# Optimization experiments

Measured on AMD Instinct MI355X. Metric: run time of the kernel, lower is better.

## Reference

```python
import jax, jax.numpy as jnp
import numpy as np


def log_g(x):
    # log of g(x) = x + 0.5 if x >= 0 else sigmoid(x)  (minGRU paper Appendix B)
    return jnp.where(x >= 0, jnp.log(jax.nn.relu(x) + 0.5), -jax.nn.softplus(-x))


def parallel_scan_log(log_coeffs, log_values):
    # log_coeffs: [B, T, H]; log_values: [B, T+1, H]
    a_star = jnp.pad(jnp.cumsum(log_coeffs, axis=1), ((0, 0), (1, 0), (0, 0)))  # [B, T+1, H]
    log_h = a_star + jax.lax.cumlogsumexp(log_values - a_star, axis=1)
    return jnp.exp(log_h)  # [B, T+1, H]


def setup_inputs() -> dict:
    key = jax.random.key(0)
    ks = jax.random.split(key, 6)
    B, T, D, H = 4, 4096, 1024, 1024
    scale = 1.0 / np.sqrt(D)
    return {
        "x": jax.random.normal(ks[0], (B, T, D), dtype=jnp.float32),
        "h_0": jax.random.uniform(ks[1], (B, H), dtype=jnp.float32),
        "Wz": jax.random.normal(ks[2], (H, D), dtype=jnp.float32) * scale,
        "bz": jnp.zeros((H,), dtype=jnp.float32),
        "Wh": jax.random.normal(ks[3], (H, D), dtype=jnp.float32) * scale,
        "bh": jnp.zeros((H,), dtype=jnp.float32),
    }


def reference(x, h_0, Wz, bz, Wh, bh):
    T = x.shape[1]
    k = jnp.einsum("btd,hd->bth", x, Wz) + bz          # linear_z(x)
    log_z = -jax.nn.softplus(-k)                          # log sigmoid(k)
    log_coeffs = -jax.nn.softplus(k)                      # log (1 - sigmoid(k))
    log_h_0 = log_g(h_0)[:, None, :]                      # [B, 1, H]
    log_tilde_h = log_g(jnp.einsum("btd,hd->bth", x, Wh) + bh)
    log_values = jnp.concatenate([log_h_0, log_z + log_tilde_h], axis=1)  # [B, T+1, H]
    h = parallel_scan_log(log_coeffs, log_values)
    return h[:, -T:, :]
```

## Files before the change

### kernel.cpp

```cpp
#include <hip/hip_runtime.h>
#include <hip/hip_bf16.h>
#include <hip/hip_fp16.h>

#define B_ 4
#define T_ 4096
#define D_ 1024
#define H_ 1024
#define M_ (B_ * T_)

typedef __attribute__((ext_vector_type(8))) short short8;
typedef __attribute__((ext_vector_type(4))) float f32x4;

__device__ __forceinline__ unsigned short f2bf(float f) {
    unsigned int u = __float_as_uint(f);
    u += 0x7fffu + ((u >> 16) & 1u);
    return (unsigned short)(u >> 16);
}

__global__ __launch_bounds__(256) void convert_all(
    const float* __restrict__ x, const float* __restrict__ wz, const float* __restrict__ wh,
    unsigned short* __restrict__ xb, unsigned short* __restrict__ wzb, unsigned short* __restrict__ whb)
{
    int i = blockIdx.x * 256 + threadIdx.x;
    const float* s; unsigned short* d; int off;
    if (i < 4194304)      { s = x;  d = xb;  off = i; }
    else if (i < 4456448) { s = wz; d = wzb; off = i - 4194304; }
    else                  { s = wh; d = whb; off = i - 4456448; }
    float4 f = ((const float4*)s)[off];
    ushort4 u;
    u.x = f2bf(f.x); u.y = f2bf(f.y); u.z = f2bf(f.z); u.w = f2bf(f.w);
    ((ushort4*)d)[off] = u;
}

__device__ __forceinline__ void async16(const void* g, void* l) {
    __builtin_amdgcn_global_load_lds(
        (__attribute__((address_space(1))) void*)g,
        (__attribute__((address_space(3))) void*)l,
        16, 0, 0);
}

__global__ __launch_bounds__(256, 4) void dual_gemm_kernel(
    const unsigned short* __restrict__ xb,
    const unsigned short* __restrict__ wzb,
    const unsigned short* __restrict__ whb,
    const float* __restrict__ bz,
    const float* __restrict__ bh,
    __half2* __restrict__ av16,
    float2* __restrict__ chunkAV)
{
    __shared__ short8 ldsA[8 * 64];
    __shared__ short8 ldsBz[4 * 64];
    __shared__ short8 ldsBh[4 * 64];

    const int tid   = threadIdx.x;
    const int lane  = tid & 63;
    const int w     = __builtin_amdgcn_readfirstlane(tid >> 6);
    const int whalf = w >> 1;
    const int nhalf = w & 1;
    const int nb    = blockIdx.x >> 7;
    const int mb    = blockIdx.x & 127;
    const int r16   = lane & 15;
    const int q     = lane >> 4;

    const int laneoff = r16 * D_ + q * 8;

    const unsigned short* gA0 = xb  + (size_t)(mb * 128 + (2 * w) * 16) * D_ + laneoff;
    const unsigned short* gA1 = gA0 + 16 * D_;
    const unsigned short* gBz = wzb + (size_t)(nb * 64 + w * 16) * D_ + laneoff;
    const unsigned short* gBh = whb + (size_t)(nb * 64 + w * 16) * D_ + laneoff;
    short8* lA0 = &ldsA[(2 * w) * 64];
    short8* lA1 = &ldsA[(2 * w + 1) * 64];
    short8* lBz = &ldsBz[w * 64];
    short8* lBh = &ldsBh[w * 64];

    f32x4 accz[4][2] = {};
    f32x4 acch[4][2] = {};

    for (int kk = 0; kk < D_; kk += 32) {
        __syncthreads();
        async16(gA0 + kk, lA0);
        async16(gA1 + kk, lA1);
        async16(gBz + kk, lBz);
        async16(gBh + kk, lBh);
        __syncthreads();

        short8 fa[4], fz[2], fh[2];
#pragma unroll
        for (int gm = 0; gm < 4; ++gm) fa[gm] = ldsA[(whalf * 4 + gm) * 64 + lane];
#pragma unroll
        for (int gn = 0; gn < 2; ++gn) {
            fz[gn] = ldsBz[(nhalf * 2 + gn) * 64 + lane];
            fh[gn] = ldsBh[(nhalf * 2 + gn) * 64 + lane];
        }
#pragma unroll
        for (int gm = 0; gm < 4; ++gm)
#pragma unroll
            for (int gn = 0; gn < 2; ++gn) {
                accz[gm][gn] = __builtin_amdgcn_mfma_f32_16x16x32_bf16(fa[gm], fz[gn], accz[gm][gn], 0, 0, 0);
                acch[gm][gn] = __builtin_amdgcn_mfma_f32_16x16x32_bf16(fa[gm], fh[gn], acch[gm][gn], 0, 0, 0);
            }
    }

    const int cglob = mb * 2 + whalf;
    const int cc = cglob & 63;
    const int bb = cglob >> 6;
#pragma unroll
    for (int gn = 0; gn < 2; ++gn) {
        const int ncol = nb * 64 + nhalf * 32 + gn * 16 + r16;
        const float bzv = bz[ncol];
        const float bhv = bh[ncol];
        float CA = 1.0f, CV = 0.0f;
#pragma unroll
        for (int gm = 0; gm < 4; ++gm) {
            float LA = 1.0f, LV = 0.0f;
#pragma unroll
            for (int rr = 0; rr < 4; ++rr) {
                float kv = accz[gm][gn][rr] + bzv;
                float hv = acch[gm][gn][rr] + bhv;
                float tk = __expf(-fabsf(kv));
                float ik = 1.0f / (1.0f + tk);
                float sig = (kv >= 0.0f) ? ik : tk * ik;
                float ac  = (kv >= 0.0f) ? tk * ik : ik;
                float th = __expf(-fabsf(hv));
                float ih = 1.0f / (1.0f + th);
                float gh = (hv >= 0.0f) ? (hv + 0.5f) : th * ih;
                float vv = sig * gh;
                const size_t m = (size_t)mb * 128 + whalf * 64 + gm * 16 + q * 4 + rr;
                av16[(size_t)m * H_ + ncol] = __floats2half2_rn(ac, vv);
                LV = ac * LV + vv;
                LA = ac * LA;
            }
#pragma unroll
            for (int mask = 16; mask <= 32; mask <<= 1) {
                float PA = __shfl_xor(LA, mask);
                float PV = __shfl_xor(LV, mask);
                if (lane & mask) { LV = LA * PV + LV; LA = LA * PA; }
                else             { LV = PA * LV + PV; LA = PA * LA; }
            }
            CV = LA * CV + LV;
            CA = LA * CA;
        }
        if (q == 0)
            chunkAV[cc * 4096 + bb * 1024 + ncol] = make_float2(CA, CV);
    }
}

__global__ __launch_bounds__(256) void scan_pass2(const float2* __restrict__ chunkAV,
                                                  const float* __restrict__ h0,
                                                  float* __restrict__ hstart) {
    int chan = blockIdx.x * blockDim.x + threadIdx.x;
    int n = chan & (H_ - 1);
    int b = chan >> 10;
    float x = h0[b * H_ + n];
    float h;
    if (x >= 0.0f) { h = x + 0.5f; }
    else { float t = __expf(x); h = t / (1.0f + t); }
#pragma unroll 8
    for (int c = 0; c < 64; ++c) {
        hstart[c * 4096 + chan] = h;
        float2 s = chunkAV[c * 4096 + chan];
        h = s.x * h + s.y;
    }
}

__global__ __launch_bounds__(256) void scan_pass3(const __half2* __restrict__ av16,
                                                  const float* __restrict__ hstart,
                                                  float* __restrict__ out) {
    int g = blockIdx.x * blockDim.x + threadIdx.x;
    int n = g & (H_ - 1);
    int rest = g >> 10;
    int c = rest & 63;
    int b = rest >> 6;
    float h = hstart[c * 4096 + b * 1024 + n];
    const __half2* base = av16 + ((size_t)(b * T_ + c * 64)) * H_ + n;
    float* obase = out + ((size_t)(b * T_ + c * 64)) * H_ + n;
#pragma unroll 8
    for (int t = 0; t < 64; ++t) {
        float2 p = __half22float2(base[(size_t)t * H_]);
        h = p.x * h + p.y;
        obase[(size_t)t * H_] = h;
    }
}

extern "C" void kernel_launch(void* const* d_in, const int* in_sizes, int n_in,
                              void* d_out, int out_size, void* d_ws, size_t ws_size,
                              hipStream_t stream) {
    const float* x  = (const float*)d_in[0];
    const float* h0 = (const float*)d_in[1];
    const float* Wz = (const float*)d_in[2];
    const float* bz = (const float*)d_in[3];
    const float* Wh = (const float*)d_in[4];
    const float* bh = (const float*)d_in[5];
    float* out = (float*)d_out;

    char* ws = (char*)d_ws;
    unsigned short* xb  = (unsigned short*)(ws);
    unsigned short* wzb = (unsigned short*)(ws + 33554432);
    unsigned short* whb = (unsigned short*)(ws + 35651584);
    __half2* av16       = (__half2*)(ws + 37748736);
    float2* chunkAV     = (float2*)(ws + 104857600);
    float*  hstart      = (float*)(ws + 106954752);

    convert_all<<<18432, 256, 0, stream>>>(x, Wz, Wh, xb, wzb, whb);

    dual_gemm_kernel<<<2048, 256, 0, stream>>>(xb, wzb, whb, bz, bh, av16, chunkAV);

    scan_pass2<<<16,   256, 0, stream>>>(chunkAV, h0, hstart);
    scan_pass3<<<1024, 256, 0, stream>>>(av16, hstart, out);
}
```

Baseline: 285.4 us.

## Double-buffer LDS in dual GEMM and enlarge block to 512 threads

The dual GEMM now uses 512-thread blocks covering 256 rows, so each B tile is shared across twice as many A rows. LDS is double-buffered so that async global-to-LDS loads for the next k-slice are issued before the MFMA work on the current one, leaving one barrier per half step. The block index mapping also changes to walk N fastest within an M block, which should help L2 reuse of the A rows. The cost is higher LDS use per block and fewer blocks, which may lower occupancy.

```diff
diff --git a/kernel.cpp b/kernel.cpp
--- a/kernel.cpp
+++ b/kernel.cpp
@@ -39,7 +39,7 @@
         16, 0, 0);
 }
 
-__global__ __launch_bounds__(256, 4) void dual_gemm_kernel(
+__global__ __launch_bounds__(512, 6) void dual_gemm_kernel(
     const unsigned short* __restrict__ xb,
     const unsigned short* __restrict__ wzb,
     const unsigned short* __restrict__ whb,
@@ -48,65 +48,73 @@
     __half2* __restrict__ av16,
     float2* __restrict__ chunkAV)
 {
-    __shared__ short8 ldsA[8 * 64];
-    __shared__ short8 ldsBz[4 * 64];
-    __shared__ short8 ldsBh[4 * 64];
-
-    const int tid   = threadIdx.x;
-    const int lane  = tid & 63;
-    const int w     = __builtin_amdgcn_readfirstlane(tid >> 6);
-    const int whalf = w >> 1;
-    const int nhalf = w & 1;
-    const int nb    = blockIdx.x >> 7;
-    const int mb    = blockIdx.x & 127;
-    const int r16   = lane & 15;
-    const int q     = lane >> 4;
+    __shared__ short8 lds[2][24 * 64];
+
+    const int tid  = threadIdx.x;
+    const int lane = tid & 63;
+    const int w    = __builtin_amdgcn_readfirstlane(tid >> 6);
+    const int mq   = w >> 1;
+    const int nh   = w & 1;
+    const int mb   = blockIdx.x >> 4;
+    const int nb   = blockIdx.x & 15;
+    const int r16  = lane & 15;
+    const int q    = lane >> 4;
 
     const int laneoff = r16 * D_ + q * 8;
-
-    const unsigned short* gA0 = xb  + (size_t)(mb * 128 + (2 * w) * 16) * D_ + laneoff;
+    const unsigned short* gA0 = xb + (size_t)(mb * 256 + (2 * w) * 16) * D_ + laneoff;
     const unsigned short* gA1 = gA0 + 16 * D_;
-    const unsigned short* gBz = wzb + (size_t)(nb * 64 + w * 16) * D_ + laneoff;
-    const unsigned short* gBh = whb + (size_t)(nb * 64 + w * 16) * D_ + laneoff;
-    short8* lA0 = &ldsA[(2 * w) * 64];
-    short8* lA1 = &ldsA[(2 * w + 1) * 64];
-    short8* lBz = &ldsBz[w * 64];
-    short8* lBh = &ldsBh[w * 64];
+    const unsigned short* gB  = (w < 4)
+        ? wzb + (size_t)(nb * 64 + w * 16) * D_ + laneoff
+        : whb + (size_t)(nb * 64 + (w - 4) * 16) * D_ + laneoff;
 
     f32x4 accz[4][2] = {};
     f32x4 acch[4][2] = {};
 
-    for (int kk = 0; kk < D_; kk += 32) {
+#define STAGE(b, koff) do {                                   \
+    async16(gA0 + (koff), &lds[b][(2 * w) * 64]);             \
+    async16(gA1 + (koff), &lds[b][(2 * w + 1) * 64]);         \
+    async16(gB  + (koff), &lds[b][(16 + w) * 64]);            \
+    } while (0)
+
+#define COMPUTE(b) do {                                                          \
+    short8 fa[4], fz[2], fh[2];                                                  \
+    _Pragma("unroll") for (int gm = 0; gm < 4; ++gm)                             \
+        fa[gm] = lds[b][(4 * mq + gm) * 64 + lane];                              \
+    _Pragma("unroll") for (int gn = 0; gn < 2; ++gn) {                           \
+        fz[gn] = lds[b][(16 + 2 * nh + gn) * 64 + lane];                         \
+        fh[gn] = lds[b][(20 + 2 * nh + gn) * 64 + lane];                         \
+    }                                                                            \
+    _Pragma("unroll") for (int gm = 0; gm < 4; ++gm)                             \
+    _Pragma("unroll") for (int gn = 0; gn < 2; ++gn) {                           \
+        accz[gm][gn] = __builtin_amdgcn_mfma_f32_16x16x32_bf16(fa[gm], fz[gn], accz[gm][gn], 0, 0, 0); \
+        acch[gm][gn] = __builtin_amdgcn_mfma_f32_16x16x32_bf16(fa[gm], fh[gn], acch[gm][gn], 0, 0, 0); \
+    } } while (0)
+
+    STAGE(0, 0);
+    int kk = 0;
+#pragma unroll 1
+    for (; kk < D_ - 64; kk += 64) {
         __syncthreads();
-        async16(gA0 + kk, lA0);
-        async16(gA1 + kk, lA1);
-        async16(gBz + kk, lBz);
-        async16(gBh + kk, lBh);
+        STAGE(1, kk + 32);
+        COMPUTE(0);
         __syncthreads();
-
-        short8 fa[4], fz[2], fh[2];
-#pragma unroll
-        for (int gm = 0; gm < 4; ++gm) fa[gm] = ldsA[(whalf * 4 + gm) * 64 + lane];
-#pragma unroll
-        for (int gn = 0; gn < 2; ++gn) {
-            fz[gn] = ldsBz[(nhalf * 2 + gn) * 64 + lane];
-            fh[gn] = ldsBh[(nhalf * 2 + gn) * 64 + lane];
-        }
-#pragma unroll
-        for (int gm = 0; gm < 4; ++gm)
-#pragma unroll
-            for (int gn = 0; gn < 2; ++gn) {
-                accz[gm][gn] = __builtin_amdgcn_mfma_f32_16x16x32_bf16(fa[gm], fz[gn], accz[gm][gn], 0, 0, 0);
-                acch[gm][gn] = __builtin_amdgcn_mfma_f32_16x16x32_bf16(fa[gm], fh[gn], acch[gm][gn], 0, 0, 0);
-            }
-    }
-
-    const int cglob = mb * 2 + whalf;
+        STAGE(0, kk + 64);
+        COMPUTE(1);
+    }
+    __syncthreads();
+    STAGE(1, kk + 32);
+    COMPUTE(0);
+    __syncthreads();
+    COMPUTE(1);
+#undef STAGE
+#undef COMPUTE
+
+    const int cglob = mb * 4 + mq;
     const int cc = cglob & 63;
     const int bb = cglob >> 6;
 #pragma unroll
     for (int gn = 0; gn < 2; ++gn) {
-        const int ncol = nb * 64 + nhalf * 32 + gn * 16 + r16;
+        const int ncol = nb * 64 + nh * 32 + gn * 16 + r16;
         const float bzv = bz[ncol];
         const float bhv = bh[ncol];
         float CA = 1.0f, CV = 0.0f;
@@ -125,7 +133,7 @@
                 float ih = 1.0f / (1.0f + th);
                 float gh = (hv >= 0.0f) ? (hv + 0.5f) : th * ih;
                 float vv = sig * gh;
-                const size_t m = (size_t)mb * 128 + whalf * 64 + gm * 16 + q * 4 + rr;
+                const size_t m = (size_t)mb * 256 + mq * 64 + gm * 16 + q * 4 + rr;
                 av16[(size_t)m * H_ + ncol] = __floats2half2_rn(ac, vv);
                 LV = ac * LV + vv;
                 LA = ac * LA;
@@ -203,7 +211,7 @@
 
     convert_all<<<18432, 256, 0, stream>>>(x, Wz, Wh, xb, wzb, whb);
 
-    dual_gemm_kernel<<<2048, 256, 0, stream>>>(xb, wzb, whb, bz, bh, av16, chunkAV);
+    dual_gemm_kernel<<<1024, 512, 0, stream>>>(xb, wzb, whb, bz, bh, av16, chunkAV);
 
     scan_pass2<<<16,   256, 0, stream>>>(chunkAV, h0, hstart);
     scan_pass3<<<1024, 256, 0, stream>>>(av16, hstart, out);
```

Measured after the change: 454.6 us. 59.3% more time.
